# Optimization experiments

Measured on AMD Instinct MI355X. Metric: run time of the kernel, lower is better.

The kernel has to match this reference:

```python
import jax, jax.numpy as jnp
import numpy as np

N = 100_000      # num nodes
E = 600_000      # num edges (before self-loops)
IN, H, C, OUT = 128, 4, 64, 1   # in_channels, heads, hidden_channels, out_channels
NEG_SLOPE = 0.2  # PyG GATConv leaky_relu slope


def setup_inputs() -> dict:
    key = jax.random.key(0)
    ks = jax.random.split(key, 12)
    init = lambda k, sh: (jax.random.normal(k, sh, jnp.float32) * 0.05)
    return {
        "x": jax.random.normal(ks[0], (N, IN), jnp.float32),
        "edge_index": jax.random.randint(ks[1], (2, E), 0, N, dtype=jnp.int32),
        # conv1: GATConv(IN -> C, heads=H, concat) -> out dim H*C
        "W1": init(ks[2], (IN, H, C)),
        "att_src1": init(ks[3], (H, C)),
        "att_dst1": init(ks[4], (H, C)),
        "b1": jnp.zeros((H * C,), jnp.float32),
        # conv2: GATConv(H*C -> C, heads=H, head-mean to match Linear(C, OUT))
        "W2": init(ks[5], (H * C, H, C)),
        "att_src2": init(ks[6], (H, C)),
        "att_dst2": init(ks[7], (H, C)),
        "b2": jnp.zeros((C,), jnp.float32),
        # PReLU (single shared parameter, torch default init 0.25)
        "prelu_a": jnp.float32(0.25),
        # level_predictor: Linear(C, OUT)
        "Wl": init(ks[8], (C, OUT)),
        "bl": jnp.zeros((OUT,), jnp.float32),
    }


def _add_self_loops(edge_index):
    loops = jnp.arange(N, dtype=edge_index.dtype)
    return jnp.concatenate([edge_index, jnp.stack([loops, loops])], axis=1)


def _gat_conv(x, src, dst, W, att_src, att_dst, bias, concat):
    # x: [N, F]; W: [F, H, C]
    h = jnp.einsum("nf,fhc->nhc", x, W)                      # [N, H, C]
    a_src = jnp.sum(h * att_src, axis=-1)                     # [N, H]
    a_dst = jnp.sum(h * att_dst, axis=-1)                     # [N, H]
    e = jax.nn.leaky_relu(a_src[src] + a_dst[dst], NEG_SLOPE)  # [Etot, H]
    # segment-softmax over incoming edges of each destination node
    m = jax.ops.segment_max(e, dst, num_segments=N)            # [N, H]
    e = jnp.exp(e - m[dst])
    denom = jax.ops.segment_sum(e, dst, num_segments=N)        # [N, H]
    alpha = e / (denom[dst] + 1e-16)                           # [Etot, H]
    out = jax.ops.segment_sum(h[src] * alpha[..., None], dst, num_segments=N)  # [N, H, C]
    out = out.reshape(N, H * C) if concat else out.mean(axis=1)
    return out + bias


def _prelu(x, a):
    return jnp.where(x >= 0, x, a * x)


def reference(x, edge_index, W1, att_src1, att_dst1, b1,
              W2, att_src2, att_dst2, b2, prelu_a, Wl, bl):
    # k-hop 'extraction' over the full node set is an identity -> full edge set.
    ei = _add_self_loops(edge_index)
    src, dst = ei[0], ei[1]
    h = _gat_conv(x, src, dst, W1, att_src1, att_dst1, b1, concat=True)   # [N, H*C]
    h = _prelu(h, prelu_a)
    h = _gat_conv(h, src, dst, W2, att_src2, att_dst2, b2, concat=False)  # [N, C]
    h = _prelu(h, prelu_a)
    return (h @ Wl + bl).squeeze(-1)                                       # [N]
```

## Files before the change

### kernel.cpp

```cpp
#include <hip/hip_runtime.h>
#include <cstdint>
#include <cstddef>

static constexpr int N_NODES = 100000;
static constexpr int N_EDGES = 600000;
static constexpr int E_TOT   = N_EDGES + N_NODES;
static constexpr float NEG_SLOPE = 0.2f;

typedef __attribute__((ext_vector_type(8))) short bf16x8;
typedef __attribute__((ext_vector_type(4))) float f32x4;
typedef __attribute__((ext_vector_type(4))) _Float16 half4;

__device__ __forceinline__ float leaky(float x) { return x >= 0.f ? x : NEG_SLOPE * x; }

__device__ __forceinline__ unsigned short f2bf(float f) {
  unsigned u = __float_as_uint(f);
  u = u + 0x7fffu + ((u >> 16) & 1u);
  return (unsigned short)(u >> 16);
}
__device__ __forceinline__ float bf2f(unsigned short h) {
  return __uint_as_float((unsigned)h << 16);
}

__device__ __forceinline__ void gload16(const unsigned short* g, unsigned short* l) {
  __builtin_amdgcn_global_load_lds(
      (const __attribute__((address_space(1))) unsigned int*)g,
      (__attribute__((address_space(3))) unsigned int*)l,
      16, 0, 0);
}


__global__ __launch_bounds__(256) void k_init_counts(int* __restrict__ counts) {
  int i = blockIdx.x * 256 + threadIdx.x;
  if (i < N_NODES) counts[i] = 1;
}

__global__ __launch_bounds__(256) void k_hist(const int* __restrict__ ei, int* __restrict__ counts) {
  int e = blockIdx.x * 256 + threadIdx.x;
  if (e < N_EDGES) atomicAdd(&counts[ei[N_EDGES + e]], 1);
}

__global__ __launch_bounds__(256) void k_scan1(const int* __restrict__ counts,
                                               int* __restrict__ partial,
                                               int* __restrict__ blockSums) {
  __shared__ int tmp[256];
  int tid = threadIdx.x;
  int i = blockIdx.x * 256 + tid;
  int v = (i < N_NODES) ? counts[i] : 0;
  tmp[tid] = v;
  __syncthreads();
  for (int off = 1; off < 256; off <<= 1) {
    int t = (tid >= off) ? tmp[tid - off] : 0;
    __syncthreads();
    tmp[tid] += t;
    __syncthreads();
  }
  if (i < N_NODES) partial[i] = tmp[tid] - v;
  if (tid == 255) blockSums[blockIdx.x] = tmp[tid];
}

__global__ __launch_bounds__(512) void k_scan2(int* __restrict__ blockSums, int nb) {
  __shared__ int tmp[512];
  int tid = threadIdx.x;
  int v = (tid < nb) ? blockSums[tid] : 0;
  tmp[tid] = v;
  __syncthreads();
  for (int off = 1; off < 512; off <<= 1) {
    int t = (tid >= off) ? tmp[tid - off] : 0;
    __syncthreads();
    tmp[tid] += t;
    __syncthreads();
  }
  if (tid < nb) blockSums[tid] = tmp[tid] - v;
}

__global__ __launch_bounds__(256) void k_scan3(const int* __restrict__ partial,
                                               const int* __restrict__ blockSums,
                                               int* __restrict__ rowptr,
                                               int* __restrict__ fill) {
  int i = blockIdx.x * 256 + threadIdx.x;
  if (i < N_NODES) {
    int v = partial[i] + blockSums[blockIdx.x];
    rowptr[i] = v;
    fill[i] = v;
  }
  if (i == 0) rowptr[N_NODES] = E_TOT;
}

__global__ __launch_bounds__(256) void k_scatter(const int* __restrict__ ei,
                                                 int* __restrict__ fill,
                                                 int* __restrict__ esrc) {
  int i = blockIdx.x * 256 + threadIdx.x;
  if (i >= E_TOT) return;
  int s, d;
  if (i < N_EDGES) { s = ei[i]; d = ei[N_EDGES + i]; }
  else             { s = i - N_EDGES; d = s; }
  int pos = atomicAdd(&fill[d], 1);
  esrc[pos] = s;
}


template <int K>
__global__ __launch_bounds__(256) void k_wconv(const float* __restrict__ W,
                                               unsigned short* __restrict__ Wt_hi,
                                               unsigned short* __restrict__ Wt_lo) {
  int t = blockIdx.x * 256 + threadIdx.x;
  if (t >= K * 256) return;
  int k = t >> 8, c = t & 255;
  float v = W[t];
  unsigned short hi = f2bf(v);
  Wt_hi[(size_t)c * K + k] = hi;
  Wt_lo[(size_t)c * K + k] = f2bf(v - bf2f(hi));
}

template <int K>
__global__ __launch_bounds__(256) void k_wa(const float* __restrict__ W,
                                            const float* __restrict__ att_s,
                                            const float* __restrict__ att_d,
                                            unsigned short* __restrict__ Wat_hi,
                                            unsigned short* __restrict__ Wat_lo) {
  int k = blockIdx.x;
  int h = threadIdx.x >> 6, c = threadIdx.x & 63;
  float wv = W[(size_t)k * 256 + h * 64 + c];
  float ps = wv * att_s[h * 64 + c];
  float pd = wv * att_d[h * 64 + c];
#pragma unroll
  for (int off = 32; off > 0; off >>= 1) {
    ps += __shfl_xor(ps, off);
    pd += __shfl_xor(pd, off);
  }
  if (c == 0) {
    unsigned short hi = f2bf(ps);
    Wat_hi[(size_t)h * K + k] = hi;
    Wat_lo[(size_t)h * K + k] = f2bf(ps - bf2f(hi));
    hi = f2bf(pd);
    Wat_hi[(size_t)(4 + h) * K + k] = hi;
    Wat_lo[(size_t)(4 + h) * K + k] = f2bf(pd - bf2f(hi));
  }
  if (threadIdx.x >= 8 && threadIdx.x < 16) {
    Wat_hi[(size_t)threadIdx.x * K + k] = 0;
    Wat_lo[(size_t)threadIdx.x * K + k] = 0;
  }
}


__global__ __launch_bounds__(256) void k_conv_x(const float* __restrict__ X,
                                                unsigned short* __restrict__ Xhi,
                                                unsigned short* __restrict__ Xlo) {
  size_t t = (size_t)blockIdx.x * 256 + threadIdx.x;
  float4 v = *(const float4*)&X[t * 4];
  ushort4 hi, lo;
  hi.x = f2bf(v.x); lo.x = f2bf(v.x - bf2f(hi.x));
  hi.y = f2bf(v.y); lo.y = f2bf(v.y - bf2f(hi.y));
  hi.z = f2bf(v.z); lo.z = f2bf(v.z - bf2f(hi.z));
  hi.w = f2bf(v.w); lo.w = f2bf(v.w - bf2f(hi.w));
  *(ushort4*)&Xhi[t * 4] = hi;
  *(ushort4*)&Xlo[t * 4] = lo;
}


template <int K>
__global__ __launch_bounds__(256, 2) void k_gemm_mfma(
    const unsigned short* __restrict__ Ahi, const unsigned short* __restrict__ Alo,
    const unsigned short* __restrict__ Bhi, const unsigned short* __restrict__ Blo,
    const unsigned short* __restrict__ Whi, const unsigned short* __restrict__ Wlo,
    _Float16* __restrict__ H, float* __restrict__ asrc, float* __restrict__ adst) {
  __shared__ __align__(16) unsigned short lds[2][20480];

  const int tid = threadIdx.x;
  const int w = tid >> 6, lane = tid & 63;
  const int lhi = lane >> 4, llo = lane & 15;
  const int wrow = blockIdx.x * 64;
  const int wcol = w * 64;

  const int sr = tid >> 2;
  const int sc = (tid & 3) ^ (sr & 3);
  int ar = wrow + sr; if (ar > N_NODES - 1) ar = N_NODES - 1;
  const unsigned short* gAh = &Ahi[(size_t)ar * K + sc * 8];
  const unsigned short* gAl = &Alo[(size_t)ar * K + sc * 8];
  const unsigned short* gB0h = &Bhi[(size_t)(0 * 64 + sr) * K + sc * 8];
  const unsigned short* gB1h = &Bhi[(size_t)(1 * 64 + sr) * K + sc * 8];
  const unsigned short* gB2h = &Bhi[(size_t)(2 * 64 + sr) * K + sc * 8];
  const unsigned short* gB3h = &Bhi[(size_t)(3 * 64 + sr) * K + sc * 8];
  const unsigned short* gB0l = &Blo[(size_t)(0 * 64 + sr) * K + sc * 8];
  const unsigned short* gB1l = &Blo[(size_t)(1 * 64 + sr) * K + sc * 8];
  const unsigned short* gB2l = &Blo[(size_t)(2 * 64 + sr) * K + sc * 8];
  const unsigned short* gB3l = &Blo[(size_t)(3 * 64 + sr) * K + sc * 8];
  const int wb = w * 512;

  const unsigned short* gWh = &Whi[(size_t)llo * K + lhi * 8];
  const unsigned short* gWl = &Wlo[(size_t)llo * K + lhi * 8];

  f32x4 acc[4][4] = {};
  f32x4 acca[4] = {};

  const int ach = (lhi ^ (llo & 3)) * 8;

  auto STAGE = [&](int buf, int kc) {
    unsigned short* L = lds[buf];
    gload16(gAh + kc, L + 0 + wb);
    gload16(gAl + kc, L + 2048 + wb);
    gload16(gB0h + kc, L + 4096 + 0 * 2048 + wb);
    gload16(gB1h + kc, L + 4096 + 1 * 2048 + wb);
    gload16(gB2h + kc, L + 4096 + 2 * 2048 + wb);
    gload16(gB3h + kc, L + 4096 + 3 * 2048 + wb);
    gload16(gB0l + kc, L + 12288 + 0 * 2048 + wb);
    gload16(gB1l + kc, L + 12288 + 1 * 2048 + wb);
    gload16(gB2l + kc, L + 12288 + 2 * 2048 + wb);
    gload16(gB3l + kc, L + 12288 + 3 * 2048 + wb);
  };

  STAGE(0, 0);
  __syncthreads();

  constexpr int NT = K / 32;
  int cur = 0;
#pragma unroll 2
  for (int t = 0; t < NT; ++t) {
    if (t + 1 < NT) STAGE(cur ^ 1, (t + 1) * 32);

    bf16x8 wh{}, wlv{};
    if (w == 0) {
      wh  = *(const bf16x8*)&gWh[t * 32];
      wlv = *(const bf16x8*)&gWl[t * 32];
    }

    const unsigned short* L = lds[cur];
    bf16x8 ah[4], al[4], bh[4], bl[4];
#pragma unroll
    for (int rt = 0; rt < 4; ++rt) {
      ah[rt] = *(const bf16x8*)&L[(rt * 16 + llo) * 32 + ach];
      al[rt] = *(const bf16x8*)&L[2048 + (rt * 16 + llo) * 32 + ach];
    }
#pragma unroll
    for (int ct = 0; ct < 4; ++ct) {
      bh[ct] = *(const bf16x8*)&L[4096 + (wcol + ct * 16 + llo) * 32 + ach];
      bl[ct] = *(const bf16x8*)&L[12288 + (wcol + ct * 16 + llo) * 32 + ach];
    }

#pragma unroll
    for (int ct = 0; ct < 4; ++ct)
#pragma unroll
      for (int rt = 0; rt < 4; ++rt) {
        acc[rt][ct] = __builtin_amdgcn_mfma_f32_16x16x32_bf16(ah[rt], bh[ct], acc[rt][ct], 0, 0, 0);
        acc[rt][ct] = __builtin_amdgcn_mfma_f32_16x16x32_bf16(al[rt], bh[ct], acc[rt][ct], 0, 0, 0);
        acc[rt][ct] = __builtin_amdgcn_mfma_f32_16x16x32_bf16(ah[rt], bl[ct], acc[rt][ct], 0, 0, 0);
      }
    if (w == 0) {
#pragma unroll
      for (int rt = 0; rt < 4; ++rt) {
        acca[rt] = __builtin_amdgcn_mfma_f32_16x16x32_bf16(ah[rt], wh, acca[rt], 0, 0, 0);
        acca[rt] = __builtin_amdgcn_mfma_f32_16x16x32_bf16(al[rt], wh, acca[rt], 0, 0, 0);
        acca[rt] = __builtin_amdgcn_mfma_f32_16x16x32_bf16(ah[rt], wlv, acca[rt], 0, 0, 0);
      }
    }
    __syncthreads();
    cur ^= 1;
  }

#pragma unroll
  for (int rt = 0; rt < 4; ++rt) {
    const int r0 = wrow + rt * 16 + lhi * 4;
#pragma unroll
    for (int ct = 0; ct < 4; ++ct) {
      const int cc = wcol + ct * 16 + llo;
#pragma unroll
      for (int e = 0; e < 4; ++e) {
        int r = r0 + e;
        if (r < N_NODES) H[(size_t)r * 256 + cc] = (_Float16)acc[rt][ct][e];
      }
    }
    if (w == 0 && llo < 8) {
#pragma unroll
      for (int e = 0; e < 4; ++e) {
        int r = r0 + e;
        if (r < N_NODES) {
          float v = acca[rt][e];
          if (llo < 4) asrc[(size_t)r * 4 + llo] = v;
          else         adst[(size_t)r * 4 + (llo - 4)] = v;
        }
      }
    }
  }
}


__global__ __launch_bounds__(256) void k_stats(const float* __restrict__ asrc,
                                               const float* __restrict__ adst,
                                               const int* __restrict__ rowptr,
                                               const int* __restrict__ esrc,
                                               float* __restrict__ pbuf,
                                               float* __restrict__ dinv) {
  int t = blockIdx.x * 256 + threadIdx.x;
  int d = t >> 2, h = t & 3;
  if (d >= N_NODES) return;
  const int beg = rowptr[d], end = rowptr[d + 1];
  const float ad = adst[(size_t)d * 4 + h];

  float m = -INFINITY;
  for (int j = beg; j < end; ++j) {
    float e = leaky(asrc[(size_t)esrc[j] * 4 + h] + ad);
    m = fmaxf(m, e);
  }
  float den = 0.f;
  for (int j = beg; j < end; ++j) {
    float p = __expf(leaky(asrc[(size_t)esrc[j] * 4 + h] + ad) - m);
    den += p;
    pbuf[(size_t)j * 4 + h] = p;
  }
  dinv[(size_t)d * 4 + h] = 1.f / (den + 1e-16f);
}


__device__ __forceinline__ float4 gather_rows(const _Float16* __restrict__ htab,
                                              const float* __restrict__ pbuf,
                                              const int* __restrict__ esrc,
                                              int beg, int end, int lane, int myh) {
  float4 acc = make_float4(0.f, 0.f, 0.f, 0.f);
  for (int w = beg; w < end; w += 16) {
    const int cnt = end - w < 16 ? end - w : 16;
    const float pl = pbuf[(size_t)w * 4 + lane];
    const int   sl = esrc[w + (lane & 15)];
    for (int c0 = 0; c0 < cnt; c0 += 4) {
      int   s0 = __shfl(sl, c0 + 0), s1 = __shfl(sl, c0 + 1);
      int   s2 = __shfl(sl, c0 + 2), s3 = __shfl(sl, c0 + 3);
      float p0 = __shfl(pl, (c0 + 0) * 4 + myh), p1 = __shfl(pl, (c0 + 1) * 4 + myh);
      float p2 = __shfl(pl, (c0 + 2) * 4 + myh), p3 = __shfl(pl, (c0 + 3) * 4 + myh);
      half4 v0{}, v1{}, v2{}, v3{};
      v0 = *(const half4*)&htab[(size_t)s0 * 256 + 4 * lane];
      if (c0 + 1 < cnt) v1 = *(const half4*)&htab[(size_t)s1 * 256 + 4 * lane]; else p1 = 0.f;
      if (c0 + 2 < cnt) v2 = *(const half4*)&htab[(size_t)s2 * 256 + 4 * lane]; else p2 = 0.f;
      if (c0 + 3 < cnt) v3 = *(const half4*)&htab[(size_t)s3 * 256 + 4 * lane]; else p3 = 0.f;
      acc.x = fmaf(p0, (float)v0[0], acc.x); acc.y = fmaf(p0, (float)v0[1], acc.y);
      acc.z = fmaf(p0, (float)v0[2], acc.z); acc.w = fmaf(p0, (float)v0[3], acc.w);
      acc.x = fmaf(p1, (float)v1[0], acc.x); acc.y = fmaf(p1, (float)v1[1], acc.y);
      acc.z = fmaf(p1, (float)v1[2], acc.z); acc.w = fmaf(p1, (float)v1[3], acc.w);
      acc.x = fmaf(p2, (float)v2[0], acc.x); acc.y = fmaf(p2, (float)v2[1], acc.y);
      acc.z = fmaf(p2, (float)v2[2], acc.z); acc.w = fmaf(p2, (float)v2[3], acc.w);
      acc.x = fmaf(p3, (float)v3[0], acc.x); acc.y = fmaf(p3, (float)v3[1], acc.y);
      acc.z = fmaf(p3, (float)v3[2], acc.z); acc.w = fmaf(p3, (float)v3[3], acc.w);
    }
  }
  return acc;
}


__global__ __launch_bounds__(256) void k_agg1(const _Float16* __restrict__ h1,
                                              const float* __restrict__ pbuf,
                                              const float* __restrict__ dinv,
                                              const int* __restrict__ rowptr,
                                              const int* __restrict__ esrc,
                                              const float* __restrict__ b1,
                                              const float* __restrict__ prelu_a,
                                              unsigned short* __restrict__ out_hi,
                                              unsigned short* __restrict__ out_lo) {
  int gid = blockIdx.x * 256 + threadIdx.x;
  int dst = gid >> 6;
  int lane = threadIdx.x & 63;
  if (dst >= N_NODES) return;
  const int beg = rowptr[dst], end = rowptr[dst + 1];
  const int myh = lane >> 4;

  float4 acc = gather_rows(h1, pbuf, esrc, beg, end, lane, myh);
  const float sc = dinv[(size_t)dst * 4 + myh];
  acc.x *= sc; acc.y *= sc; acc.z *= sc; acc.w *= sc;

  const float a = prelu_a[0];
  const int c = 4 * lane;
  const float4 bv = *(const float4*)&b1[c];
  float4 r;
  r.x = acc.x + bv.x; r.x = r.x >= 0.f ? r.x : a * r.x;
  r.y = acc.y + bv.y; r.y = r.y >= 0.f ? r.y : a * r.y;
  r.z = acc.z + bv.z; r.z = r.z >= 0.f ? r.z : a * r.z;
  r.w = acc.w + bv.w; r.w = r.w >= 0.f ? r.w : a * r.w;

  ushort4 hi, lo;
  hi.x = f2bf(r.x); lo.x = f2bf(r.x - bf2f(hi.x));
  hi.y = f2bf(r.y); lo.y = f2bf(r.y - bf2f(hi.y));
  hi.z = f2bf(r.z); lo.z = f2bf(r.z - bf2f(hi.z));
  hi.w = f2bf(r.w); lo.w = f2bf(r.w - bf2f(hi.w));
  *(ushort4*)&out_hi[(size_t)dst * 256 + c] = hi;
  *(ushort4*)&out_lo[(size_t)dst * 256 + c] = lo;
}


__global__ __launch_bounds__(256) void k_agg2(const _Float16* __restrict__ h2,
                                              const float* __restrict__ pbuf,
                                              const float* __restrict__ dinv,
                                              const int* __restrict__ rowptr,
                                              const int* __restrict__ esrc,
                                              const float* __restrict__ b2,
                                              const float* __restrict__ prelu_a,
                                              const float* __restrict__ Wl,
                                              const float* __restrict__ bl,
                                              float* __restrict__ out) {
  int gid = blockIdx.x * 256 + threadIdx.x;
  int dst = gid >> 6;
  int lane = threadIdx.x & 63;
  if (dst >= N_NODES) return;
  const int beg = rowptr[dst], end = rowptr[dst + 1];
  const int myh = lane >> 4;

  float4 acc = gather_rows(h2, pbuf, esrc, beg, end, lane, myh);
  const float sc = dinv[(size_t)dst * 4 + myh];
  acc.x *= sc; acc.y *= sc; acc.z *= sc; acc.w *= sc;

#pragma unroll
  for (int off = 16; off < 64; off <<= 1) {
    acc.x += __shfl_xor(acc.x, off);
    acc.y += __shfl_xor(acc.y, off);
    acc.z += __shfl_xor(acc.z, off);
    acc.w += __shfl_xor(acc.w, off);
  }

  const float a = prelu_a[0];
  const int c0 = 4 * (lane & 15);
  float4 v;
  v.x = 0.25f * acc.x + b2[c0 + 0]; v.x = v.x >= 0.f ? v.x : a * v.x;
  v.y = 0.25f * acc.y + b2[c0 + 1]; v.y = v.y >= 0.f ? v.y : a * v.y;
  v.z = 0.25f * acc.z + b2[c0 + 2]; v.z = v.z >= 0.f ? v.z : a * v.z;
  v.w = 0.25f * acc.w + b2[c0 + 3]; v.w = v.w >= 0.f ? v.w : a * v.w;

  float p = v.x * Wl[c0 + 0] + v.y * Wl[c0 + 1] + v.z * Wl[c0 + 2] + v.w * Wl[c0 + 3];
#pragma unroll
  for (int off = 1; off < 16; off <<= 1) p += __shfl_xor(p, off);

  if (lane == 0) out[dst] = p + bl[0];
}


static inline int cdiv(int a, int b) { return (a + b - 1) / b; }

extern "C" void kernel_launch(void* const* d_in, const int* in_sizes, int n_in,
                              void* d_out, int out_size, void* d_ws, size_t ws_size,
                              hipStream_t stream) {
  const float* x   = (const float*)d_in[0];
  const int*   ei  = (const int*)d_in[1];
  const float* W1  = (const float*)d_in[2];
  const float* as1 = (const float*)d_in[3];
  const float* ad1 = (const float*)d_in[4];
  const float* b1  = (const float*)d_in[5];
  const float* W2  = (const float*)d_in[6];
  const float* as2 = (const float*)d_in[7];
  const float* ad2 = (const float*)d_in[8];
  const float* b2  = (const float*)d_in[9];
  const float* pa  = (const float*)d_in[10];
  const float* Wl  = (const float*)d_in[11];
  const float* bl  = (const float*)d_in[12];
  float* out = (float*)d_out;

  char* ws = (char*)d_ws;
  size_t off = 0;
  auto alloc = [&](size_t bytes) -> void* {
    void* p = ws + off;
    off += (bytes + 255) & ~(size_t)255;
    return p;
  };

  _Float16* hbufA = (_Float16*)alloc((size_t)N_NODES * 256 * sizeof(_Float16));
  unsigned short* R1 = (unsigned short*)alloc((size_t)N_NODES * 256 * 2 * sizeof(unsigned short));
  unsigned short* x_hi   = R1;
  unsigned short* x_lo   = R1 + (size_t)N_NODES * 128;
  unsigned short* h1p_hi = R1;
  unsigned short* h1p_lo = R1 + (size_t)N_NODES * 256;

  float* asrc1 = (float*)alloc((size_t)N_NODES * 4 * sizeof(float));
  float* adst1 = (float*)alloc((size_t)N_NODES * 4 * sizeof(float));
  float* asrc2 = (float*)alloc((size_t)N_NODES * 4 * sizeof(float));
  float* adst2 = (float*)alloc((size_t)N_NODES * 4 * sizeof(float));
  float* pbuf  = (float*)alloc(((size_t)E_TOT * 4 + 64) * sizeof(float));
  float* dinv  = (float*)alloc((size_t)N_NODES * 4 * sizeof(float));

  unsigned short* Wt1_hi  = (unsigned short*)alloc(256 * 128 * sizeof(unsigned short));
  unsigned short* Wt1_lo  = (unsigned short*)alloc(256 * 128 * sizeof(unsigned short));
  unsigned short* Wat1_hi = (unsigned short*)alloc(16 * 128 * sizeof(unsigned short));
  unsigned short* Wat1_lo = (unsigned short*)alloc(16 * 128 * sizeof(unsigned short));
  unsigned short* Wt2_hi  = (unsigned short*)alloc(256 * 256 * sizeof(unsigned short));
  unsigned short* Wt2_lo  = (unsigned short*)alloc(256 * 256 * sizeof(unsigned short));
  unsigned short* Wat2_hi = (unsigned short*)alloc(16 * 256 * sizeof(unsigned short));
  unsigned short* Wat2_lo = (unsigned short*)alloc(16 * 256 * sizeof(unsigned short));

  int* counts  = (int*)alloc((size_t)N_NODES * sizeof(int));
  int* partial = (int*)alloc((size_t)N_NODES * sizeof(int));
  int* rowptr  = (int*)alloc((size_t)(N_NODES + 1) * sizeof(int));
  int* fill    = (int*)alloc((size_t)N_NODES * sizeof(int));
  int* esrc    = (int*)alloc(((size_t)E_TOT + 64) * sizeof(int));
  int* blockSums = (int*)alloc(2048 * sizeof(int));

  const int NB = cdiv(N_NODES, 256);

  k_init_counts<<<NB, 256, 0, stream>>>(counts);
  k_hist<<<cdiv(N_EDGES, 256), 256, 0, stream>>>(ei, counts);
  k_scan1<<<NB, 256, 0, stream>>>(counts, partial, blockSums);
  k_scan2<<<1, 512, 0, stream>>>(blockSums, NB);
  k_scan3<<<NB, 256, 0, stream>>>(partial, blockSums, rowptr, fill);
  k_scatter<<<cdiv(E_TOT, 256), 256, 0, stream>>>(ei, fill, esrc);

  k_wconv<128><<<cdiv(128 * 256, 256), 256, 0, stream>>>(W1, Wt1_hi, Wt1_lo);
  k_wa<128><<<128, 256, 0, stream>>>(W1, as1, ad1, Wat1_hi, Wat1_lo);
  k_wconv<256><<<cdiv(256 * 256, 256), 256, 0, stream>>>(W2, Wt2_hi, Wt2_lo);
  k_wa<256><<<256, 256, 0, stream>>>(W2, as2, ad2, Wat2_hi, Wat2_lo);

  k_conv_x<<<N_NODES * 128 / 4 / 256, 256, 0, stream>>>(x, x_hi, x_lo);

  const int GEMM_GRID = cdiv(N_NODES, 64);
  const int STATS_GRID = cdiv(N_NODES * 4, 256);

  k_gemm_mfma<128><<<GEMM_GRID, 256, 0, stream>>>(x_hi, x_lo, Wt1_hi, Wt1_lo,
                                                  Wat1_hi, Wat1_lo, hbufA, asrc1, adst1);
  k_stats<<<STATS_GRID, 256, 0, stream>>>(asrc1, adst1, rowptr, esrc, pbuf, dinv);
  k_agg1<<<N_NODES * 64 / 256, 256, 0, stream>>>(hbufA, pbuf, dinv, rowptr, esrc,
                                                 b1, pa, h1p_hi, h1p_lo);

  k_gemm_mfma<256><<<GEMM_GRID, 256, 0, stream>>>(h1p_hi, h1p_lo, Wt2_hi, Wt2_lo,
                                                  Wat2_hi, Wat2_lo, hbufA, asrc2, adst2);
  k_stats<<<STATS_GRID, 256, 0, stream>>>(asrc2, adst2, rowptr, esrc, pbuf, dinv);
  k_agg2<<<N_NODES * 64 / 256, 256, 0, stream>>>(hbufA, pbuf, dinv, rowptr, esrc,
                                                 b2, pa, Wl, bl, out);
}
```

Before: 356.5 us.

## Replace split-bf16 three-pass GEMM with single-pass fp16 MFMA

Drops the hi/lo bf16 split emulation of fp32 (three MFMAs per tile) and uses one fp16 MFMA pass with fp16-converted inputs, weights and layer-1 outputs. This cuts MFMA work by about two thirds, halves the staged LDS and global traffic for operands, and raises the occupancy hint to 3 blocks per CU. The cost is lower precision: fp16 has an 11-bit mantissa and limited range, so GEMM accuracy is reduced compared with the near-fp32 split scheme.

After: 303.5 us. -14.9%, faster.

```diff
diff --git a/kernel.cpp b/kernel.cpp
--- a/kernel.cpp
+++ b/kernel.cpp
@@ -7,22 +7,13 @@
 static constexpr int E_TOT   = N_EDGES + N_NODES;
 static constexpr float NEG_SLOPE = 0.2f;
 
-typedef __attribute__((ext_vector_type(8))) short bf16x8;
+typedef __attribute__((ext_vector_type(8))) _Float16 f16x8;
 typedef __attribute__((ext_vector_type(4))) float f32x4;
 typedef __attribute__((ext_vector_type(4))) _Float16 half4;
 
 __device__ __forceinline__ float leaky(float x) { return x >= 0.f ? x : NEG_SLOPE * x; }
 
-__device__ __forceinline__ unsigned short f2bf(float f) {
-  unsigned u = __float_as_uint(f);
-  u = u + 0x7fffu + ((u >> 16) & 1u);
-  return (unsigned short)(u >> 16);
-}
-__device__ __forceinline__ float bf2f(unsigned short h) {
-  return __uint_as_float((unsigned)h << 16);
-}
-
-__device__ __forceinline__ void gload16(const unsigned short* g, unsigned short* l) {
+__device__ __forceinline__ void gload16(const void* g, void* l) {
   __builtin_amdgcn_global_load_lds(
       (const __attribute__((address_space(1))) unsigned int*)g,
       (__attribute__((address_space(3))) unsigned int*)l,
@@ -102,23 +93,18 @@
 
 template <int K>
 __global__ __launch_bounds__(256) void k_wconv(const float* __restrict__ W,
-                                               unsigned short* __restrict__ Wt_hi,
-                                               unsigned short* __restrict__ Wt_lo) {
+                                               _Float16* __restrict__ Wt) {
   int t = blockIdx.x * 256 + threadIdx.x;
   if (t >= K * 256) return;
   int k = t >> 8, c = t & 255;
-  float v = W[t];
-  unsigned short hi = f2bf(v);
-  Wt_hi[(size_t)c * K + k] = hi;
-  Wt_lo[(size_t)c * K + k] = f2bf(v - bf2f(hi));
+  Wt[(size_t)c * K + k] = (_Float16)W[t];
 }
 
 template <int K>
 __global__ __launch_bounds__(256) void k_wa(const float* __restrict__ W,
                                             const float* __restrict__ att_s,
                                             const float* __restrict__ att_d,
-                                            unsigned short* __restrict__ Wat_hi,
-                                            unsigned short* __restrict__ Wat_lo) {
+                                            _Float16* __restrict__ Wat) {
   int k = blockIdx.x;
   int h = threadIdx.x >> 6, c = threadIdx.x & 63;
   float wv = W[(size_t)k * 256 + h * 64 + c];
@@ -130,42 +116,31 @@
     pd += __shfl_xor(pd, off);
   }
   if (c == 0) {
-    unsigned short hi = f2bf(ps);
-    Wat_hi[(size_t)h * K + k] = hi;
-    Wat_lo[(size_t)h * K + k] = f2bf(ps - bf2f(hi));
-    hi = f2bf(pd);
-    Wat_hi[(size_t)(4 + h) * K + k] = hi;
-    Wat_lo[(size_t)(4 + h) * K + k] = f2bf(pd - bf2f(hi));
-  }
-  if (threadIdx.x >= 8 && threadIdx.x < 16) {
-    Wat_hi[(size_t)threadIdx.x * K + k] = 0;
-    Wat_lo[(size_t)threadIdx.x * K + k] = 0;
-  }
+    Wat[(size_t)h * K + k] = (_Float16)ps;
+    Wat[(size_t)(4 + h) * K + k] = (_Float16)pd;
+  }
+  if (threadIdx.x >= 8 && threadIdx.x < 16)
+    Wat[(size_t)threadIdx.x * K + k] = (_Float16)0.f;
 }
 
 
 __global__ __launch_bounds__(256) void k_conv_x(const float* __restrict__ X,
-                                                unsigned short* __restrict__ Xhi,
-                                                unsigned short* __restrict__ Xlo) {
+                                                _Float16* __restrict__ X16) {
   size_t t = (size_t)blockIdx.x * 256 + threadIdx.x;
   float4 v = *(const float4*)&X[t * 4];
-  ushort4 hi, lo;
-  hi.x = f2bf(v.x); lo.x = f2bf(v.x - bf2f(hi.x));
-  hi.y = f2bf(v.y); lo.y = f2bf(v.y - bf2f(hi.y));
-  hi.z = f2bf(v.z); lo.z = f2bf(v.z - bf2f(hi.z));
-  hi.w = f2bf(v.w); lo.w = f2bf(v.w - bf2f(hi.w));
-  *(ushort4*)&Xhi[t * 4] = hi;
-  *(ushort4*)&Xlo[t * 4] = lo;
+  half4 o;
+  o[0] = (_Float16)v.x; o[1] = (_Float16)v.y;
+  o[2] = (_Float16)v.z; o[3] = (_Float16)v.w;
+  *(half4*)&X16[t * 4] = o;
 }
 
 
 template <int K>
-__global__ __launch_bounds__(256, 2) void k_gemm_mfma(
-    const unsigned short* __restrict__ Ahi, const unsigned short* __restrict__ Alo,
-    const unsigned short* __restrict__ Bhi, const unsigned short* __restrict__ Blo,
-    const unsigned short* __restrict__ Whi, const unsigned short* __restrict__ Wlo,
+__global__ __launch_bounds__(256, 3) void k_gemm_mfma(
+    const _Float16* __restrict__ A, const _Float16* __restrict__ B,
+    const _Float16* __restrict__ Wa,
     _Float16* __restrict__ H, float* __restrict__ asrc, float* __restrict__ adst) {
-  __shared__ __align__(16) unsigned short lds[2][20480];
+  __shared__ __align__(16) _Float16 lds[2][10240];
 
   const int tid = threadIdx.x;
   const int w = tid >> 6, lane = tid & 63;
@@ -176,20 +151,14 @@
   const int sr = tid >> 2;
   const int sc = (tid & 3) ^ (sr & 3);
   int ar = wrow + sr; if (ar > N_NODES - 1) ar = N_NODES - 1;
-  const unsigned short* gAh = &Ahi[(size_t)ar * K + sc * 8];
-  const unsigned short* gAl = &Alo[(size_t)ar * K + sc * 8];
-  const unsigned short* gB0h = &Bhi[(size_t)(0 * 64 + sr) * K + sc * 8];
-  const unsigned short* gB1h = &Bhi[(size_t)(1 * 64 + sr) * K + sc * 8];
-  const unsigned short* gB2h = &Bhi[(size_t)(2 * 64 + sr) * K + sc * 8];
-  const unsigned short* gB3h = &Bhi[(size_t)(3 * 64 + sr) * K + sc * 8];
-  const unsigned short* gB0l = &Blo[(size_t)(0 * 64 + sr) * K + sc * 8];
-  const unsigned short* gB1l = &Blo[(size_t)(1 * 64 + sr) * K + sc * 8];
-  const unsigned short* gB2l = &Blo[(size_t)(2 * 64 + sr) * K + sc * 8];
-  const unsigned short* gB3l = &Blo[(size_t)(3 * 64 + sr) * K + sc * 8];
+  const _Float16* gA  = &A[(size_t)ar * K + sc * 8];
+  const _Float16* gB0 = &B[(size_t)(0 * 64 + sr) * K + sc * 8];
+  const _Float16* gB1 = &B[(size_t)(1 * 64 + sr) * K + sc * 8];
+  const _Float16* gB2 = &B[(size_t)(2 * 64 + sr) * K + sc * 8];
+  const _Float16* gB3 = &B[(size_t)(3 * 64 + sr) * K + sc * 8];
   const int wb = w * 512;
 
-  const unsigned short* gWh = &Whi[(size_t)llo * K + lhi * 8];
-  const unsigned short* gWl = &Wlo[(size_t)llo * K + lhi * 8];
+  const _Float16* gW = &Wa[(size_t)llo * K + lhi * 8];
 
   f32x4 acc[4][4] = {};
   f32x4 acca[4] = {};
@@ -197,17 +166,12 @@
   const int ach = (lhi ^ (llo & 3)) * 8;
 
   auto STAGE = [&](int buf, int kc) {
-    unsigned short* L = lds[buf];
-    gload16(gAh + kc, L + 0 + wb);
-    gload16(gAl + kc, L + 2048 + wb);
-    gload16(gB0h + kc, L + 4096 + 0 * 2048 + wb);
-    gload16(gB1h + kc, L + 4096 + 1 * 2048 + wb);
-    gload16(gB2h + kc, L + 4096 + 2 * 2048 + wb);
-    gload16(gB3h + kc, L + 4096 + 3 * 2048 + wb);
-    gload16(gB0l + kc, L + 12288 + 0 * 2048 + wb);
-    gload16(gB1l + kc, L + 12288 + 1 * 2048 + wb);
-    gload16(gB2l + kc, L + 12288 + 2 * 2048 + wb);
-    gload16(gB3l + kc, L + 12288 + 3 * 2048 + wb);
+    _Float16* L = lds[buf];
+    gload16(gA + kc,  L + 0    + wb);
+    gload16(gB0 + kc, L + 2048 + wb);
+    gload16(gB1 + kc, L + 4096 + wb);
+    gload16(gB2 + kc, L + 6144 + wb);
+    gload16(gB3 + kc, L + 8192 + wb);
   };
 
   STAGE(0, 0);
@@ -219,40 +183,27 @@
   for (int t = 0; t < NT; ++t) {
     if (t + 1 < NT) STAGE(cur ^ 1, (t + 1) * 32);
 
-    bf16x8 wh{}, wlv{};
+    f16x8 wfrag{};
+    if (w == 0) wfrag = *(const f16x8*)&gW[t * 32];
+
+    const _Float16* L = lds[cur];
+    f16x8 af[4], bf[4];
+#pragma unroll
+    for (int rt = 0; rt < 4; ++rt)
+      af[rt] = *(const f16x8*)&L[(rt * 16 + llo) * 32 + ach];
+#pragma unroll
+    for (int ct = 0; ct < 4; ++ct)
+      bf[ct] = *(const f16x8*)&L[2048 + (wcol + ct * 16 + llo) * 32 + ach];
+
+#pragma unroll
+    for (int ct = 0; ct < 4; ++ct)
+#pragma unroll
+      for (int rt = 0; rt < 4; ++rt)
+        acc[rt][ct] = __builtin_amdgcn_mfma_f32_16x16x32_f16(af[rt], bf[ct], acc[rt][ct], 0, 0, 0);
     if (w == 0) {
-      wh  = *(const bf16x8*)&gWh[t * 32];
-      wlv = *(const bf16x8*)&gWl[t * 32];
-    }
-
-    const unsigned short* L = lds[cur];
-    bf16x8 ah[4], al[4], bh[4], bl[4];
-#pragma unroll
-    for (int rt = 0; rt < 4; ++rt) {
-      ah[rt] = *(const bf16x8*)&L[(rt * 16 + llo) * 32 + ach];
-      al[rt] = *(const bf16x8*)&L[2048 + (rt * 16 + llo) * 32 + ach];
-    }
-#pragma unroll
-    for (int ct = 0; ct < 4; ++ct) {
-      bh[ct] = *(const bf16x8*)&L[4096 + (wcol + ct * 16 + llo) * 32 + ach];
-      bl[ct] = *(const bf16x8*)&L[12288 + (wcol + ct * 16 + llo) * 32 + ach];
-    }
-
-#pragma unroll
-    for (int ct = 0; ct < 4; ++ct)
-#pragma unroll
-      for (int rt = 0; rt < 4; ++rt) {
-        acc[rt][ct] = __builtin_amdgcn_mfma_f32_16x16x32_bf16(ah[rt], bh[ct], acc[rt][ct], 0, 0, 0);
-        acc[rt][ct] = __builtin_amdgcn_mfma_f32_16x16x32_bf16(al[rt], bh[ct], acc[rt][ct], 0, 0, 0);
-        acc[rt][ct] = __builtin_amdgcn_mfma_f32_16x16x32_bf16(ah[rt], bl[ct], acc[rt][ct], 0, 0, 0);
-      }
-    if (w == 0) {
-#pragma unroll
-      for (int rt = 0; rt < 4; ++rt) {
-        acca[rt] = __builtin_amdgcn_mfma_f32_16x16x32_bf16(ah[rt], wh, acca[rt], 0, 0, 0);
-        acca[rt] = __builtin_amdgcn_mfma_f32_16x16x32_bf16(al[rt], wh, acca[rt], 0, 0, 0);
-        acca[rt] = __builtin_amdgcn_mfma_f32_16x16x32_bf16(ah[rt], wlv, acca[rt], 0, 0, 0);
-      }
+#pragma unroll
+      for (int rt = 0; rt < 4; ++rt)
+        acca[rt] = __builtin_amdgcn_mfma_f32_16x16x32_f16(af[rt], wfrag, acca[rt], 0, 0, 0);
     }
     __syncthreads();
     cur ^= 1;
@@ -352,8 +303,7 @@
                                               const int* __restrict__ esrc,
                                               const float* __restrict__ b1,
                                               const float* __restrict__ prelu_a,
-                                              unsigned short* __restrict__ out_hi,
-                                              unsigned short* __restrict__ out_lo) {
+                                              _Float16* __restrict__ outp) {
   int gid = blockIdx.x * 256 + threadIdx.x;
   int dst = gid >> 6;
   int lane = threadIdx.x & 63;
@@ -374,13 +324,10 @@
   r.z = acc.z + bv.z; r.z = r.z >= 0.f ? r.z : a * r.z;
   r.w = acc.w + bv.w; r.w = r.w >= 0.f ? r.w : a * r.w;
 
-  ushort4 hi, lo;
-  hi.x = f2bf(r.x); lo.x = f2bf(r.x - bf2f(hi.x));
-  hi.y = f2bf(r.y); lo.y = f2bf(r.y - bf2f(hi.y));
-  hi.z = f2bf(r.z); lo.z = f2bf(r.z - bf2f(hi.z));
-  hi.w = f2bf(r.w); lo.w = f2bf(r.w - bf2f(hi.w));
-  *(ushort4*)&out_hi[(size_t)dst * 256 + c] = hi;
-  *(ushort4*)&out_lo[(size_t)dst * 256 + c] = lo;
+  half4 o;
+  o[0] = (_Float16)r.x; o[1] = (_Float16)r.y;
+  o[2] = (_Float16)r.z; o[3] = (_Float16)r.w;
+  *(half4*)&outp[(size_t)dst * 256 + c] = o;
 }
 
 
@@ -458,11 +405,9 @@
   };
 
   _Float16* hbufA = (_Float16*)alloc((size_t)N_NODES * 256 * sizeof(_Float16));
-  unsigned short* R1 = (unsigned short*)alloc((size_t)N_NODES * 256 * 2 * sizeof(unsigned short));
-  unsigned short* x_hi   = R1;
-  unsigned short* x_lo   = R1 + (size_t)N_NODES * 128;
-  unsigned short* h1p_hi = R1;
-  unsigned short* h1p_lo = R1 + (size_t)N_NODES * 256;
+  _Float16* R1 = (_Float16*)alloc((size_t)N_NODES * 256 * sizeof(_Float16));
+  _Float16* x16  = R1;
+  _Float16* h1p  = R1;
 
   float* asrc1 = (float*)alloc((size_t)N_NODES * 4 * sizeof(float));
   float* adst1 = (float*)alloc((size_t)N_NODES * 4 * sizeof(float));
@@ -471,14 +416,10 @@
   float* pbuf  = (float*)alloc(((size_t)E_TOT * 4 + 64) * sizeof(float));
   float* dinv  = (float*)alloc((size_t)N_NODES * 4 * sizeof(float));
 
-  unsigned short* Wt1_hi  = (unsigned short*)alloc(256 * 128 * sizeof(unsigned short));
-  unsigned short* Wt1_lo  = (unsigned short*)alloc(256 * 128 * sizeof(unsigned short));
-  unsigned short* Wat1_hi = (unsigned short*)alloc(16 * 128 * sizeof(unsigned short));
-  unsigned short* Wat1_lo = (unsigned short*)alloc(16 * 128 * sizeof(unsigned short));
-  unsigned short* Wt2_hi  = (unsigned short*)alloc(256 * 256 * sizeof(unsigned short));
-  unsigned short* Wt2_lo  = (unsigned short*)alloc(256 * 256 * sizeof(unsigned short));
-  unsigned short* Wat2_hi = (unsigned short*)alloc(16 * 256 * sizeof(unsigned short));
-  unsigned short* Wat2_lo = (unsigned short*)alloc(16 * 256 * sizeof(unsigned short));
+  _Float16* Wt1  = (_Float16*)alloc(256 * 128 * sizeof(_Float16));
+  _Float16* Wat1 = (_Float16*)alloc(16 * 128 * sizeof(_Float16));
+  _Float16* Wt2  = (_Float16*)alloc(256 * 256 * sizeof(_Float16));
+  _Float16* Wat2 = (_Float16*)alloc(16 * 256 * sizeof(_Float16));
 
   int* counts  = (int*)alloc((size_t)N_NODES * sizeof(int));
   int* partial = (int*)alloc((size_t)N_NODES * sizeof(int));
@@ -496,24 +437,22 @@
   k_scan3<<<NB, 256, 0, stream>>>(partial, blockSums, rowptr, fill);
   k_scatter<<<cdiv(E_TOT, 256), 256, 0, stream>>>(ei, fill, esrc);
 
-  k_wconv<128><<<cdiv(128 * 256, 256), 256, 0, stream>>>(W1, Wt1_hi, Wt1_lo);
-  k_wa<128><<<128, 256, 0, stream>>>(W1, as1, ad1, Wat1_hi, Wat1_lo);
-  k_wconv<256><<<cdiv(256 * 256, 256), 256, 0, stream>>>(W2, Wt2_hi, Wt2_lo);
-  k_wa<256><<<256, 256, 0, stream>>>(W2, as2, ad2, Wat2_hi, Wat2_lo);
-
-  k_conv_x<<<N_NODES * 128 / 4 / 256, 256, 0, stream>>>(x, x_hi, x_lo);
+  k_wconv<128><<<cdiv(128 * 256, 256), 256, 0, stream>>>(W1, Wt1);
+  k_wa<128><<<128, 256, 0, stream>>>(W1, as1, ad1, Wat1);
+  k_wconv<256><<<cdiv(256 * 256, 256), 256, 0, stream>>>(W2, Wt2);
+  k_wa<256><<<256, 256, 0, stream>>>(W2, as2, ad2, Wat2);
+
+  k_conv_x<<<N_NODES * 128 / 4 / 256, 256, 0, stream>>>(x, x16);
 
   const int GEMM_GRID = cdiv(N_NODES, 64);
   const int STATS_GRID = cdiv(N_NODES * 4, 256);
 
-  k_gemm_mfma<128><<<GEMM_GRID, 256, 0, stream>>>(x_hi, x_lo, Wt1_hi, Wt1_lo,
-                                                  Wat1_hi, Wat1_lo, hbufA, asrc1, adst1);
+  k_gemm_mfma<128><<<GEMM_GRID, 256, 0, stream>>>(x16, Wt1, Wat1, hbufA, asrc1, adst1);
   k_stats<<<STATS_GRID, 256, 0, stream>>>(asrc1, adst1, rowptr, esrc, pbuf, dinv);
   k_agg1<<<N_NODES * 64 / 256, 256, 0, stream>>>(hbufA, pbuf, dinv, rowptr, esrc,
-                                                 b1, pa, h1p_hi, h1p_lo);
-
-  k_gemm_mfma<256><<<GEMM_GRID, 256, 0, stream>>>(h1p_hi, h1p_lo, Wt2_hi, Wt2_lo,
-                                                  Wat2_hi, Wat2_lo, hbufA, asrc2, adst2);
+                                                 b1, pa, h1p);
+
+  k_gemm_mfma<256><<<GEMM_GRID, 256, 0, stream>>>(h1p, Wt2, Wat2, hbufA, asrc2, adst2);
   k_stats<<<STATS_GRID, 256, 0, stream>>>(asrc2, adst2, rowptr, esrc, pbuf, dinv);
   k_agg2<<<N_NODES * 64 / 256, 256, 0, stream>>>(hbufA, pbuf, dinv, rowptr, esrc,
                                                  b2, pa, Wl, bl, out);
```
